# Optimization experiments

Hardware: AMD Instinct MI355X
Metric: run time of the kernel (lower is better)

The kernel has to match this reference:

```python
import jax, jax.numpy as jnp
import numpy as np

N_NODES = 100000
N_EDGES = 3200000
HIDDEN = 64
IN_DIM = 3


def setup_inputs() -> dict:
    key = jax.random.key(0)
    ks = jax.random.split(key, 12)
    x = jax.random.normal(ks[0], (N_NODES, IN_DIM), dtype=jnp.float32)
    edge_index = jax.random.randint(ks[1], (2, N_EDGES), 0, N_NODES, dtype=jnp.int64)
    s1 = 1.0 / np.sqrt(IN_DIM)
    s2 = 1.0 / np.sqrt(HIDDEN)
    s3 = 1.0 / np.sqrt(2 * HIDDEN)
    return {
        "x": x,
        "edge_index": edge_index,
        # GCNConv 1: 3 -> 64
        "W1": jax.random.uniform(ks[2], (IN_DIM, HIDDEN), jnp.float32, -s1, s1),
        "b1": jnp.zeros((HIDDEN,), jnp.float32),
        # GCNConv 2: 64 -> 64
        "W2": jax.random.uniform(ks[3], (HIDDEN, HIDDEN), jnp.float32, -s2, s2),
        "b2": jnp.zeros((HIDDEN,), jnp.float32),
        # edge MLP: Linear(128,64) -> ReLU -> Linear(64,1)
        "W3": jax.random.uniform(ks[4], (2 * HIDDEN, HIDDEN), jnp.float32, -s3, s3),
        "b3": jax.random.uniform(ks[5], (HIDDEN,), jnp.float32, -s3, s3),
        "W4": jax.random.uniform(ks[6], (HIDDEN, 1), jnp.float32, -s2, s2),
        "b4": jax.random.uniform(ks[7], (1,), jnp.float32, -s2, s2),
    }


def _gcn_conv(h, W, b, row, col, n_nodes):
    """PyG GCNConv: add self-loops, symmetric D^-1/2 (A+I) D^-1/2 normalization,
    aggregate messages from source (row) at target (col)."""
    hw = h @ W  # [N, out]
    loop = jnp.arange(n_nodes, dtype=row.dtype)
    r = jnp.concatenate([row, loop])
    c = jnp.concatenate([col, loop])
    deg = jax.ops.segment_sum(jnp.ones(c.shape[0], h.dtype), c, num_segments=n_nodes)
    dinv = jnp.where(deg > 0, jax.lax.rsqrt(deg), 0.0).astype(h.dtype)
    norm = dinv[r] * dinv[c]  # [E+N]
    out = jax.ops.segment_sum(norm[:, None] * hw[r], c, num_segments=n_nodes)
    return out + b


def reference(x, edge_index, W1, b1, W2, b2, W3, b3, W4, b4):
    n_nodes = x.shape[0]
    row, col = edge_index[0], edge_index[1]
    h = jax.nn.relu(_gcn_conv(x, W1, b1, row, col, n_nodes))
    h = jax.nn.relu(_gcn_conv(h, W2, b2, row, col, n_nodes))
    # edge scorer: gather endpoints, concat, small MLP
    edge_feat = jnp.concatenate([h[row], h[col]], axis=1)  # [E, 2*hidden]
    z = jax.nn.relu(edge_feat @ W3 + b3)
    return (z @ W4 + b4).reshape(-1)  # [E]
```

## Files before the change

kernel.cpp:

```cpp
#include <hip/hip_runtime.h>

__device__ __forceinline__ float bcast_lane(float v, int lane) {
    return __int_as_float(__builtin_amdgcn_readlane(__float_as_int(v), lane));
}

__global__ void k_histr8(const int* __restrict__ col, int* __restrict__ deg8,
                         int* __restrict__ rank, int E, int N) {
    int e = blockIdx.x * 256 + threadIdx.x;
    if (e < E) {
        int r = blockIdx.x & 7;
        rank[e] = atomicAdd(&deg8[(size_t)r * N + col[e]], 1);
    }
}

__global__ void k_subbase(int* __restrict__ deg8, int* __restrict__ deg, int N) {
    int i = blockIdx.x * 256 + threadIdx.x;
    if (i >= N) return;
    int running = 0;
#pragma unroll
    for (int x = 0; x < 8; x++) {
        size_t idx = (size_t)x * N + i;
        int t = deg8[idx];
        deg8[idx] = running;
        running += t;
    }
    deg[i] = running;
}

__global__ void k_scan1(const int* __restrict__ deg, int* __restrict__ part,
                        int* __restrict__ bsum, int N) {
    __shared__ int sm[256];
    int t = threadIdx.x;
    int i = blockIdx.x * 256 + t;
    int v = (i < N) ? deg[i] : 0;
    sm[t] = v;
    __syncthreads();
    for (int d = 1; d < 256; d <<= 1) {
        int add = (t >= d) ? sm[t - d] : 0;
        __syncthreads();
        sm[t] += add;
        __syncthreads();
    }
    if (i < N) part[i] = sm[t] - v;
    if (t == 255) bsum[blockIdx.x] = sm[255];
}

__global__ void k_scan2(int* __restrict__ bsum, int nb) {
    __shared__ int sm[512];
    int t = threadIdx.x;
    int v = (t < nb) ? bsum[t] : 0;
    sm[t] = v;
    __syncthreads();
    for (int d = 1; d < 512; d <<= 1) {
        int add = (t >= d) ? sm[t - d] : 0;
        __syncthreads();
        sm[t] += add;
        __syncthreads();
    }
    if (t < nb) bsum[t] = sm[t] - v;
}

__global__ void k_scan3d(const int* __restrict__ part, const int* __restrict__ bsum,
                         const int* __restrict__ deg, const float* __restrict__ x,
                         int* __restrict__ off, float* __restrict__ dinv,
                         float4* __restrict__ y4, int N, int E) {
    int i = blockIdx.x * 256 + threadIdx.x;
    if (i < N) {
        int o = part[i] + bsum[blockIdx.x];
        off[i] = o;
        float d = rsqrtf((float)deg[i] + 1.0f);
        dinv[i] = d;
        y4[i] = make_float4(d * x[i * 3 + 0], d * x[i * 3 + 1], d * x[i * 3 + 2], 0.f);
    }
    if (i == 0) off[N] = E;
}

__global__ void k_pos8(const int* __restrict__ col, const int* __restrict__ rank,
                       const int* __restrict__ off, const int* __restrict__ sub,
                       int* __restrict__ pos, int E, int N) {
    int e = blockIdx.x * 256 + threadIdx.x;
    if (e < E) {
        int c = col[e];
        int r = (e >> 8) & 7;
        pos[e] = off[c] + sub[(size_t)r * N + c] + rank[e];
    }
}

__global__ void k_fillr(const int* __restrict__ row, const int* __restrict__ pos,
                        int* __restrict__ rowlist, int E) {
    int r = blockIdx.x & 7;
    int chunk = blockIdx.x >> 3;
    int nchunks = gridDim.x >> 3;
    int plo = (int)((long long)E * r >> 3);
    int phi = (int)((long long)E * (r + 1) >> 3);
    long long c0 = (long long)E * chunk / nchunks;
    long long c1 = (long long)E * (chunk + 1) / nchunks;
    for (long long e = c0 + threadIdx.x; e < c1; e += blockDim.x) {
        int p = __builtin_nontemporal_load(&pos[e]);
        if (p >= plo && p < phi)
            rowlist[p] = __builtin_nontemporal_load(&row[e]);
    }
}

__global__ void k_layer12(const float4* __restrict__ y4, const int* __restrict__ off,
                          const int* __restrict__ rowlist, const float* __restrict__ dinv,
                          const float* __restrict__ W1, const float* __restrict__ b1,
                          const float* __restrict__ W2, float* __restrict__ g2, int N) {
    __shared__ float W2l[4096];
    __shared__ float W1l[192];
    int tid = threadIdx.x;
    for (int i = tid; i < 4096; i += 256) W2l[i] = W2[i];
    if (tid < 192) W1l[tid] = W1[tid];
    __syncthreads();
    int wave = tid >> 6, lane = tid & 63;
    int n = blockIdx.x * 4 + wave;
    if (n >= N) return;
    int s = off[n], epos = off[n + 1];
    float ax, ay, az;
    {
        float4 self = y4[n];
        ax = (lane == 0) ? self.x : 0.f;
        ay = (lane == 0) ? self.y : 0.f;
        az = (lane == 0) ? self.z : 0.f;
    }
    for (int j = s + lane; j < epos; j += 64) {
        float4 t = y4[rowlist[j]];
        ax += t.x; ay += t.y; az += t.z;
    }
#pragma unroll
    for (int d = 1; d < 64; d <<= 1) {
        ax += __shfl_xor(ax, d);
        ay += __shfl_xor(ay, d);
        az += __shfl_xor(az, d);
    }
    float dn = dinv[n];
    float h1 = fmaxf(fmaf(dn, ax * W1l[lane] + ay * W1l[64 + lane] + az * W1l[128 + lane],
                          b1[lane]), 0.0f);
    float acc2 = 0.f;
#pragma unroll
    for (int k = 0; k < 64; k++) {
        float hk = bcast_lane(h1, k);
        acc2 = fmaf(hk, W2l[k * 64 + lane], acc2);
    }
    g2[(size_t)n * 64 + lane] = dn * acc2;
}

__global__ void k_gather(const float* __restrict__ g, const int* __restrict__ off,
                         const int* __restrict__ rl, const float* __restrict__ dinv,
                         const float* __restrict__ b, float* __restrict__ h, int N) {
    int tid = threadIdx.x;
    int wave = tid >> 6, lane = tid & 63;
    int n = blockIdx.x * 4 + wave;
    if (n >= N) return;
    int s = off[n], epos = off[n + 1];
    float a0 = g[(size_t)n * 64 + lane];
    float a1 = 0.f, a2 = 0.f, a3 = 0.f;
    float a4 = 0.f, a5 = 0.f, a6 = 0.f, a7 = 0.f;
    int j = s;
    for (; j + 7 < epos; j += 8) {
        int r0 = rl[j],     r1 = rl[j + 1], r2 = rl[j + 2], r3 = rl[j + 3];
        int r4 = rl[j + 4], r5 = rl[j + 5], r6 = rl[j + 6], r7 = rl[j + 7];
        a0 += g[(size_t)r0 * 64 + lane];
        a1 += g[(size_t)r1 * 64 + lane];
        a2 += g[(size_t)r2 * 64 + lane];
        a3 += g[(size_t)r3 * 64 + lane];
        a4 += g[(size_t)r4 * 64 + lane];
        a5 += g[(size_t)r5 * 64 + lane];
        a6 += g[(size_t)r6 * 64 + lane];
        a7 += g[(size_t)r7 * 64 + lane];
    }
    for (; j < epos; j++) a1 += g[(size_t)rl[j] * 64 + lane];
    float acc = ((a0 + a1) + (a2 + a3)) + ((a4 + a5) + (a6 + a7));
    h[(size_t)n * 64 + lane] = fmaxf(fmaf(dinv[n], acc, b[lane]), 0.0f);
}

__global__ void k_lin3(float* __restrict__ h, const float* __restrict__ W3,
                       const float* __restrict__ b3, float* __restrict__ u, int N) {
    __shared__ float Wa[4096];
    __shared__ float Wb[4096];
    int tid = threadIdx.x;
    for (int i = tid; i < 4096; i += 256) {
        Wa[i] = W3[i];
        Wb[i] = W3[4096 + i];
    }
    __syncthreads();
    int wave = tid >> 6, lane = tid & 63;
    int gid = blockIdx.x * 4 + wave;
    int stride = gridDim.x * 4;
    float bb = b3[lane];
    for (int n = gid; n < N; n += stride) {
        float hv = h[(size_t)n * 64 + lane];
        float ua = bb, va = 0.f;
#pragma unroll
        for (int k = 0; k < 64; k++) {
            float hk = bcast_lane(hv, k);
            ua = fmaf(hk, Wa[k * 64 + lane], ua);
            va = fmaf(hk, Wb[k * 64 + lane], va);
        }
        u[(size_t)n * 64 + lane] = ua;
        h[(size_t)n * 64 + lane] = va;
    }
}

__global__ void k_edge_csr(const float4* __restrict__ u4, const float4* __restrict__ v4,
                           const int* __restrict__ off, const int* __restrict__ rowlist,
                           const float4* __restrict__ w44, const float* __restrict__ b4,
                           float* __restrict__ tmp, int N) {
    int tid = threadIdx.x;
    int wave = tid >> 6, lane = tid & 63;
    int n = blockIdx.x * 4 + wave;
    if (n >= N) return;
    int c16 = lane & 15, grp = lane >> 4;
    int s = off[n], epos = off[n + 1];
    float4 vv = v4[(size_t)n * 16 + c16];
    float4 w = w44[c16];
    float bb = b4[0];
    for (int j0 = s; j0 < epos; j0 += 16) {
        int ja = j0 + grp, jb = j0 + 4 + grp, jc = j0 + 8 + grp, jd = j0 + 12 + grp;
        bool va_ = ja < epos, vb_ = jb < epos, vc_ = jc < epos, vd_ = jd < epos;
        int ra = va_ ? rowlist[ja] : 0;
        int rb = vb_ ? rowlist[jb] : 0;
        int rc = vc_ ? rowlist[jc] : 0;
        int rd = vd_ ? rowlist[jd] : 0;
        float4 a = u4[(size_t)ra * 16 + c16];
        float4 b = u4[(size_t)rb * 16 + c16];
        float4 c = u4[(size_t)rc * 16 + c16];
        float4 d = u4[(size_t)rd * 16 + c16];
        float sa = fmaxf(a.x + vv.x, 0.f) * w.x + fmaxf(a.y + vv.y, 0.f) * w.y +
                   fmaxf(a.z + vv.z, 0.f) * w.z + fmaxf(a.w + vv.w, 0.f) * w.w;
        float sb = fmaxf(b.x + vv.x, 0.f) * w.x + fmaxf(b.y + vv.y, 0.f) * w.y +
                   fmaxf(b.z + vv.z, 0.f) * w.z + fmaxf(b.w + vv.w, 0.f) * w.w;
        float sc = fmaxf(c.x + vv.x, 0.f) * w.x + fmaxf(c.y + vv.y, 0.f) * w.y +
                   fmaxf(c.z + vv.z, 0.f) * w.z + fmaxf(c.w + vv.w, 0.f) * w.w;
        float sd = fmaxf(d.x + vv.x, 0.f) * w.x + fmaxf(d.y + vv.y, 0.f) * w.y +
                   fmaxf(d.z + vv.z, 0.f) * w.z + fmaxf(d.w + vv.w, 0.f) * w.w;
        sa += __shfl_xor(sa, 1); sa += __shfl_xor(sa, 2);
        sa += __shfl_xor(sa, 4); sa += __shfl_xor(sa, 8);
        sb += __shfl_xor(sb, 1); sb += __shfl_xor(sb, 2);
        sb += __shfl_xor(sb, 4); sb += __shfl_xor(sb, 8);
        sc += __shfl_xor(sc, 1); sc += __shfl_xor(sc, 2);
        sc += __shfl_xor(sc, 4); sc += __shfl_xor(sc, 8);
        sd += __shfl_xor(sd, 1); sd += __shfl_xor(sd, 2);
        sd += __shfl_xor(sd, 4); sd += __shfl_xor(sd, 8);
        if (c16 == 0) {
            if (va_) tmp[ja] = sa + bb;
            if (vb_) tmp[jb] = sb + bb;
            if (vc_) tmp[jc] = sc + bb;
            if (vd_) tmp[jd] = sd + bb;
        }
    }
}

__global__ void k_perm(const float* __restrict__ tmp, const int* __restrict__ pos,
                       float* __restrict__ out, int E) {
    int e = blockIdx.x * blockDim.x + threadIdx.x;
    if (e < E) out[e] = tmp[pos[e]];
}

extern "C" void kernel_launch(void* const* d_in, const int* in_sizes, int n_in,
                              void* d_out, int out_size, void* d_ws, size_t ws_size,
                              hipStream_t stream) {
    const float* x  = (const float*)d_in[0];
    const int*   ei = (const int*)d_in[1];
    const float* W1 = (const float*)d_in[2];
    const float* b1 = (const float*)d_in[3];
    const float* W2 = (const float*)d_in[4];
    const float* b2 = (const float*)d_in[5];
    const float* W3 = (const float*)d_in[6];
    const float* b3 = (const float*)d_in[7];
    const float* W4 = (const float*)d_in[8];
    const float* b4 = (const float*)d_in[9];
    int N = in_sizes[0] / 3;
    int E = in_sizes[1] / 2;
    const int* row = ei;
    const int* col = ei + E;
    float* out = (float*)d_out;

    char* ws = (char*)d_ws;
    size_t off_b = 0;
    auto alloc = [&](size_t bytes) {
        void* p = ws + off_b;
        off_b += (bytes + 255) & ~(size_t)255;
        return p;
    };
    float* dinv    = (float*)alloc((size_t)N * 4);
    int*   offs    = (int*)alloc((size_t)(N + 1) * 4);
    int*   bsum    = (int*)alloc(512 * 4);
    float* bufA    = (float*)alloc((size_t)N * 64 * 4);
    float* bufB    = (float*)alloc((size_t)N * 64 * 4);
    int*   rowlist = (int*)alloc((size_t)E * 4);
    int*   pos     = (int*)alloc((size_t)E * 4);
    float* tmp     = (float*)alloc((size_t)E * 4);

    int* part = (int*)bufA;
    int* deg  = (int*)bufA + N;
    int* deg8 = (int*)bufA + 2 * N;
    float4* y4  = (float4*)bufB;
    int*   rank = (int*)bufB + (size_t)4 * N;

    dim3 B(256);
    int nbN     = (N + 255) / 256;
    int nbE     = (E + 255) / 256;
    int nbNode4 = (N + 3) / 4;

    (void)hipMemsetAsync(deg8, 0, (size_t)8 * N * 4, stream);
    k_histr8<<<nbE, B, 0, stream>>>(col, deg8, rank, E, N);
    k_subbase<<<nbN, B, 0, stream>>>(deg8, deg, N);
    k_scan1<<<nbN, B, 0, stream>>>(deg, part, bsum, N);
    k_scan2<<<1, 512, 0, stream>>>(bsum, nbN);
    k_scan3d<<<nbN, B, 0, stream>>>(part, bsum, deg, x, offs, dinv, y4, N, E);
    k_pos8<<<nbE, B, 0, stream>>>(col, rank, offs, deg8, pos, E, N);
    k_fillr<<<2048, B, 0, stream>>>(row, pos, rowlist, E);

    k_layer12<<<nbNode4, B, 0, stream>>>(y4, offs, rowlist, dinv, W1, b1, W2, bufA, N);
    k_gather<<<nbNode4, B, 0, stream>>>(bufA, offs, rowlist, dinv, b2, bufB, N);
    k_lin3<<<1280, B, 0, stream>>>(bufB, W3, b3, bufA, N);
    k_edge_csr<<<nbNode4, B, 0, stream>>>((const float4*)bufA, (const float4*)bufB,
                                          offs, rowlist, (const float4*)W4, b4, tmp, N);
    k_perm<<<nbE, B, 0, stream>>>(tmp, pos, out, E);
}
```

Measured before the change: 654.5 us.

## Replace global-atomic degree histogram with LDS-local per-range chunk histograms

The global atomic histogram over 8 replicated degree arrays is replaced by a block-local shared-memory histogram. Each of 256 blocks owns one edge chunk (of 32) and one node range (of 8), counts matching edges in LDS, and writes per-chunk counts. A prefix pass over 32 chunks then gives stable positions, and the memset disappears. In exchange, each block rescans its whole edge chunk (col is read 8 times), the count array grows to 32*N ints, and only 256 blocks run, which may limit parallelism.

```diff
diff --git a/kernel.cpp b/kernel.cpp
--- a/kernel.cpp
+++ b/kernel.cpp
@@ -4,24 +4,40 @@
     return __int_as_float(__builtin_amdgcn_readlane(__float_as_int(v), lane));
 }
 
-__global__ void k_histr8(const int* __restrict__ col, int* __restrict__ deg8,
-                         int* __restrict__ rank, int E, int N) {
-    int e = blockIdx.x * 256 + threadIdx.x;
-    if (e < E) {
-        int r = blockIdx.x & 7;
-        rank[e] = atomicAdd(&deg8[(size_t)r * N + col[e]], 1);
-    }
-}
-
-__global__ void k_subbase(int* __restrict__ deg8, int* __restrict__ deg, int N) {
+#define NCHUNK 32
+#define NRANGE 8
+#define MAXRANGE 12800
+
+__global__ void k_lhist(const int* __restrict__ col, int* __restrict__ lrank,
+                        int* __restrict__ gcounts, int E, int N) {
+    __shared__ int cnt[MAXRANGE];
+    int j = blockIdx.x & 31, r = blockIdx.x >> 5;
+    int lo = (int)((long long)N * r >> 3);
+    int hi = (int)((long long)N * (r + 1) >> 3);
+    int len = hi - lo;
+    for (int i = threadIdx.x; i < len; i += 256) cnt[i] = 0;
+    __syncthreads();
+    long long c0 = (long long)E * j / NCHUNK;
+    long long c1 = (long long)E * (j + 1) / NCHUNK;
+    for (long long e = c0 + threadIdx.x; e < c1; e += 256) {
+        int c = col[e];
+        if (c >= lo && c < hi)
+            lrank[e] = atomicAdd(&cnt[c - lo], 1);
+    }
+    __syncthreads();
+    for (int i = threadIdx.x; i < len; i += 256)
+        gcounts[(size_t)j * N + lo + i] = cnt[i];
+}
+
+__global__ void k_gbase(int* __restrict__ gcounts, int* __restrict__ deg, int N) {
     int i = blockIdx.x * 256 + threadIdx.x;
     if (i >= N) return;
     int running = 0;
 #pragma unroll
-    for (int x = 0; x < 8; x++) {
-        size_t idx = (size_t)x * N + i;
-        int t = deg8[idx];
-        deg8[idx] = running;
+    for (int j = 0; j < NCHUNK; j++) {
+        size_t idx = (size_t)j * N + i;
+        int t = gcounts[idx];
+        gcounts[idx] = running;
         running += t;
     }
     deg[i] = running;
@@ -75,14 +91,14 @@
     if (i == 0) off[N] = E;
 }
 
-__global__ void k_pos8(const int* __restrict__ col, const int* __restrict__ rank,
-                       const int* __restrict__ off, const int* __restrict__ sub,
+__global__ void k_posL(const int* __restrict__ col, const int* __restrict__ lrank,
+                       const int* __restrict__ off, const int* __restrict__ gc,
                        int* __restrict__ pos, int E, int N) {
     int e = blockIdx.x * 256 + threadIdx.x;
     if (e < E) {
         int c = col[e];
-        int r = (e >> 8) & 7;
-        pos[e] = off[c] + sub[(size_t)r * N + c] + rank[e];
+        int j = (int)((32LL * e) / E);
+        pos[e] = off[c] + gc[(size_t)j * N + c] + lrank[e];
     }
 }
 
@@ -292,24 +308,23 @@
     int*   pos     = (int*)alloc((size_t)E * 4);
     float* tmp     = (float*)alloc((size_t)E * 4);
 
-    int* part = (int*)bufA;
-    int* deg  = (int*)bufA + N;
-    int* deg8 = (int*)bufA + 2 * N;
-    float4* y4  = (float4*)bufB;
-    int*   rank = (int*)bufB + (size_t)4 * N;
+    int* part    = (int*)bufA;
+    int* deg     = (int*)bufA + N;
+    int* gcounts = (int*)bufA + 2 * N;
+    float4* y4   = (float4*)bufB;
+    int*   lrank = (int*)bufB + (size_t)4 * N;
 
     dim3 B(256);
     int nbN     = (N + 255) / 256;
     int nbE     = (E + 255) / 256;
     int nbNode4 = (N + 3) / 4;
 
-    (void)hipMemsetAsync(deg8, 0, (size_t)8 * N * 4, stream);
-    k_histr8<<<nbE, B, 0, stream>>>(col, deg8, rank, E, N);
-    k_subbase<<<nbN, B, 0, stream>>>(deg8, deg, N);
+    k_lhist<<<NRANGE * NCHUNK, B, 0, stream>>>(col, lrank, gcounts, E, N);
+    k_gbase<<<nbN, B, 0, stream>>>(gcounts, deg, N);
     k_scan1<<<nbN, B, 0, stream>>>(deg, part, bsum, N);
     k_scan2<<<1, 512, 0, stream>>>(bsum, nbN);
     k_scan3d<<<nbN, B, 0, stream>>>(part, bsum, deg, x, offs, dinv, y4, N, E);
-    k_pos8<<<nbE, B, 0, stream>>>(col, rank, offs, deg8, pos, E, N);
+    k_posL<<<nbE, B, 0, stream>>>(col, lrank, offs, gcounts, pos, E, N);
     k_fillr<<<2048, B, 0, stream>>>(row, pos, rowlist, E);
 
     k_layer12<<<nbNode4, B, 0, stream>>>(y4, offs, rowlist, dinv, W1, b1, W2, bufA, N);
```

Result: no change. 648.6 us (-0.9%).
